# Performance work log

Hardware: AMD Instinct MI355X
Metric: run time of the kernel (lower is better)

Reference implementation:

```python
import jax, jax.numpy as jnp
import numpy as np

NUM_HEADS = 16
D_ATT = 64


def setup_inputs() -> dict:
    key = jax.random.key(0)
    ks = jax.random.split(key, 7)
    b, n, hd = 4, 2048, NUM_HEADS * 64  # input last dim = num_heads * per-head embed_dim
    Q_vec = jax.random.normal(ks[0], (b, n, hd), dtype=jnp.float32)
    K_vec = jax.random.normal(ks[1], (b, n, hd), dtype=jnp.float32)
    V_vec = jax.random.normal(ks[2], (b, n, hd), dtype=jnp.float32)
    # torch Linear weights: [out_features, in_features] = [d_attention, per_head_dim]
    W_Q = jax.random.normal(ks[3], (D_ATT, 64), dtype=jnp.float32) * 0.02
    W_K = jax.random.normal(ks[4], (D_ATT, 64), dtype=jnp.float32) * 0.02
    W_V = jax.random.normal(ks[5], (D_ATT, 64), dtype=jnp.float32) * 0.02
    mask = jax.random.bernoulli(ks[6], p=0.9, shape=(b, n))  # bool [b, n]
    return {"Q_vec": Q_vec, "K_vec": K_vec, "V_vec": V_vec,
            "W_Q": W_Q, "W_K": W_K, "W_V": W_V, "mask": mask}


def reference(Q_vec, K_vec, V_vec, W_Q, W_K, W_V, mask):
    b, n, _ = Q_vec.shape
    h = NUM_HEADS
    scaling = 1.0 / np.sqrt(D_ATT).astype(np.float32)

    def split_heads(x):  # b n (h d) -> b h n d
        return x.reshape(b, n, h, -1).transpose(0, 2, 1, 3)

    # Linear applied per-head (weights are [out, in]; y = x @ W^T)
    q = split_heads(Q_vec) @ W_Q.T  # [b,h,n,D_ATT]
    k = split_heads(K_vec) @ W_K.T
    v = split_heads(V_vec) @ W_V.T

    dots = jnp.einsum('bhid,bhjd->bhij', q, k) * scaling  # [b,h,n,n]
    pair_mask = mask[:, None, :] & mask[:, :, None]       # [b,n,n]
    mask_value = -jnp.finfo(dots.dtype).max
    dots = jnp.where(pair_mask[:, None, :, :], dots, mask_value)
    attn = jax.nn.softmax(dots, axis=-1)
    out = jnp.einsum('bhij,bhjd->bhid', attn, v)          # [b,h,n,D_ATT]
    return out.transpose(0, 2, 1, 3).reshape(b, n, h * D_ATT)
```

## Files before the change

kernel.cpp:

```cpp
#include <hip/hip_runtime.h>

#define B_  4
#define N_  2048
#define H_  16
#define HD_ 1024

typedef short  bf16x8 __attribute__((ext_vector_type(8)));
typedef short  bf16x4 __attribute__((ext_vector_type(4)));
typedef float  f32x4  __attribute__((ext_vector_type(4)));

static __device__ __forceinline__ unsigned short f2bf(float f) {
    unsigned int u = __builtin_bit_cast(unsigned int, f);
    return (unsigned short)((u + 0x8000u) >> 16);
}
static __device__ __forceinline__ unsigned f2bf2pack(float lo, float hi) {
    unsigned a = __builtin_bit_cast(unsigned, lo) + 0x8000u;
    unsigned b = __builtin_bit_cast(unsigned, hi) + 0x8000u;
    return __builtin_amdgcn_perm(b, a, 0x07060302u);
}

__global__ __launch_bounds__(256) void wconv_kernel(
    const float* __restrict__ WQ, const float* __restrict__ WK,
    const float* __restrict__ WV, unsigned short* __restrict__ wbf)
{
    const int p = blockIdx.x;
    const float* W = (p == 0) ? WQ : (p == 1) ? WK : WV;
    const float scl = (p == 0) ? 0.180336880f : 1.f;
    const int t = threadIdx.x;
    const float* src = W + t * 16;
    unsigned short* dst = wbf + p * 4096 + t * 16;
    float4 f[4];
    #pragma unroll
    for (int i = 0; i < 4; ++i) f[i] = *reinterpret_cast<const float4*>(src + i * 4);
    uint4 o0, o1;
    o0.x = f2bf2pack(f[0].x * scl, f[0].y * scl);
    o0.y = f2bf2pack(f[0].z * scl, f[0].w * scl);
    o0.z = f2bf2pack(f[1].x * scl, f[1].y * scl);
    o0.w = f2bf2pack(f[1].z * scl, f[1].w * scl);
    o1.x = f2bf2pack(f[2].x * scl, f[2].y * scl);
    o1.y = f2bf2pack(f[2].z * scl, f[2].w * scl);
    o1.z = f2bf2pack(f[3].x * scl, f[3].y * scl);
    o1.w = f2bf2pack(f[3].z * scl, f[3].w * scl);
    *reinterpret_cast<uint4*>(dst)     = o0;
    *reinterpret_cast<uint4*>(dst + 8) = o1;
}

__global__ __launch_bounds__(256) void proj_kernel(
    const float* __restrict__ Qv, const float* __restrict__ Kv,
    const float* __restrict__ Vv, const unsigned short* __restrict__ wbf,
    unsigned short* __restrict__ qs, unsigned short* __restrict__ ks,
    unsigned short* __restrict__ vt)
{
    __shared__ __align__(16) unsigned short sb[64][72];

    const int tid  = threadIdx.x;
    const int wq   = tid >> 6;
    const int lane = tid & 63;
    const int l15  = lane & 15;
    const int quad = lane >> 4;

    const int i0 = blockIdx.x * 64;
    const int h  = blockIdx.y;
    const int bz = blockIdx.z;
    const int b  = bz / 3;
    const int p  = bz - b * 3;

    const size_t bh = (size_t)b * H_ + h;
    const float* inp = ((p == 0) ? Qv : (p == 1) ? Kv : Vv)
                       + ((size_t)b * N_ + i0) * HD_ + h * 64;

    const unsigned short* wb = wbf + p * 4096;
    bf16x8 bw[4][2];
    #pragma unroll
    for (int t = 0; t < 4; ++t)
        #pragma unroll
        for (int kh = 0; kh < 2; ++kh)
            bw[t][kh] = *reinterpret_cast<const bf16x8*>(wb + (t * 16 + l15) * 64 + kh * 32 + quad * 8);

    const float* xp = inp + (size_t)(wq * 16 + l15) * HD_;
    bf16x8 ax[2];
    #pragma unroll
    for (int kh = 0; kh < 2; ++kh) {
        float4 f0 = *reinterpret_cast<const float4*>(xp + kh * 32 + quad * 8);
        float4 f1 = *reinterpret_cast<const float4*>(xp + kh * 32 + quad * 8 + 4);
        uint4 u = uint4{f2bf2pack(f0.x, f0.y), f2bf2pack(f0.z, f0.w),
                        f2bf2pack(f1.x, f1.y), f2bf2pack(f1.z, f1.w)};
        ax[kh] = __builtin_bit_cast(bf16x8, u);
    }

    f32x4 C[4];
    #pragma unroll
    for (int t = 0; t < 4; ++t) {
        C[t] = f32x4{0.f, 0.f, 0.f, 0.f};
        #pragma unroll
        for (int kh = 0; kh < 2; ++kh)
            C[t] = __builtin_amdgcn_mfma_f32_16x16x32_bf16(ax[kh], bw[t][kh], C[t], 0, 0, 0);
    }

    if (p < 2) {
        #pragma unroll
        for (int t = 0; t < 4; ++t)
            #pragma unroll
            for (int r = 0; r < 4; ++r)
                sb[wq * 16 + quad * 4 + r][t * 16 + l15] = f2bf(C[t][r]);
        __syncthreads();
        unsigned short* dst = ((p == 0) ? qs : ks) + ((size_t)bh * N_ + i0) * 64;
        #pragma unroll
        for (int v = 0; v < 2; ++v) {
            int idx = tid + v * 256;
            int row = idx >> 3, c0 = (idx & 7) * 8;
            *reinterpret_cast<uint4*>(dst + (size_t)row * 64 + c0) =
                *reinterpret_cast<const uint4*>(&sb[row][c0]);
        }
    } else {
        #pragma unroll
        for (int t = 0; t < 4; ++t) {
            uint2 u;
            u.x = f2bf2pack(C[t][0], C[t][1]);
            u.y = f2bf2pack(C[t][2], C[t][3]);
            *reinterpret_cast<uint2*>(&sb[t * 16 + l15][wq * 16 + quad * 4]) = u;
        }
        __syncthreads();
        unsigned short* vdst = vt + (size_t)bh * 64 * N_ + i0;
        #pragma unroll
        for (int v = 0; v < 2; ++v) {
            int idx = tid + v * 256;
            int d = idx >> 3, c0 = (idx & 7) * 8;
            *reinterpret_cast<uint4*>(vdst + (size_t)d * N_ + c0) =
                *reinterpret_cast<const uint4*>(&sb[d][c0]);
        }
    }
}

__global__ __launch_bounds__(256, 2) void attn_kernel(
    const unsigned short* __restrict__ qs, const unsigned short* __restrict__ ks,
    const unsigned short* __restrict__ vt, const int* __restrict__ maskp,
    float* __restrict__ out)
{
    __shared__ __align__(16) unsigned short Ks[64][72];
    __shared__ __align__(16) unsigned short Vt[64][68];
    __shared__ float kb[64];

    const int tid  = threadIdx.x;
    const int w    = tid >> 6;
    const int lane = tid & 63;
    const int l15  = lane & 15;
    const int quad = lane >> 4;

    const int i0 = blockIdx.x * 256;
    const int bh = blockIdx.y;
    const int b  = bh >> 4;
    const int h  = bh & 15;
    const int qrow0 = i0 + w * 64;

    bf16x8 aq[4][2];
    float  qm[4];
    #pragma unroll
    for (int rt = 0; rt < 4; ++rt) {
        const unsigned short* qrow = qs + ((size_t)bh * N_ + qrow0 + rt * 16 + l15) * 64;
        aq[rt][0] = *reinterpret_cast<const bf16x8*>(qrow + quad * 8);
        aq[rt][1] = *reinterpret_cast<const bf16x8*>(qrow + 32 + quad * 8);
        qm[rt] = maskp[b * N_ + qrow0 + rt * 16 + l15] ? 1.f : 0.f;
    }

    bf16x8 aones;
    #pragma unroll
    for (int j = 0; j < 8; ++j) aones[j] = (short)0x3F80;

    f32x4 O[4][4];
    f32x4 L[4];
    #pragma unroll
    for (int rt = 0; rt < 4; ++rt) {
        L[rt] = f32x4{0.f, 0.f, 0.f, 0.f};
        #pragma unroll
        for (int c = 0; c < 4; ++c) O[rt][c] = f32x4{0.f, 0.f, 0.f, 0.f};
    }

    const unsigned short* kbase = ks + (size_t)bh * N_ * 64;
    const unsigned short* vbase = vt + (size_t)bh * 64 * N_;

    for (int kv0 = 0; kv0 < N_; kv0 += 64) {
        __syncthreads();
        #pragma unroll
        for (int it = 0; it < 2; ++it) {
            int idx = tid + it * 256;
            int r = idx >> 3, g = idx & 7;
            *reinterpret_cast<uint4*>(&Ks[r][g * 8]) =
                *reinterpret_cast<const uint4*>(kbase + (size_t)(kv0 + r) * 64 + g * 8);
        }
        #pragma unroll
        for (int it = 0; it < 4; ++it) {
            int idx = tid + it * 256;
            int r = idx >> 4, g2 = idx & 15;
            *reinterpret_cast<uint2*>(&Vt[r][g2 * 4]) =
                *reinterpret_cast<const uint2*>(vbase + (size_t)r * N_ + kv0 + g2 * 4);
        }
        if (tid < 64) kb[tid] = maskp[b * N_ + kv0 + tid] ? 0.f : -1e30f;
        __syncthreads();

        bf16x8 ak[4][2];
        #pragma unroll
        for (int ct = 0; ct < 4; ++ct)
            #pragma unroll
            for (int kh = 0; kh < 2; ++kh)
                ak[ct][kh] = *reinterpret_cast<const bf16x8*>(&Ks[ct * 16 + l15][kh * 32 + quad * 8]);

        bf16x8 av[4][2];
        #pragma unroll
        for (int ct = 0; ct < 4; ++ct)
            #pragma unroll
            for (int kh = 0; kh < 2; ++kh) {
                bf16x4 lo = *reinterpret_cast<const bf16x4*>(&Vt[ct * 16 + l15][kh * 32 + quad * 4]);
                bf16x4 hi = *reinterpret_cast<const bf16x4*>(&Vt[ct * 16 + l15][kh * 32 + 16 + quad * 4]);
                av[ct][kh] = bf16x8{lo[0], lo[1], lo[2], lo[3], hi[0], hi[1], hi[2], hi[3]};
            }

        f32x4 kbv[4];
        #pragma unroll
        for (int ct = 0; ct < 4; ++ct)
            kbv[ct] = *reinterpret_cast<const f32x4*>(&kb[ct * 16 + quad * 4]);

        #pragma unroll
        for (int rt = 0; rt < 4; ++rt) {
            f32x4 S[4];
            #pragma unroll
            for (int ct = 0; ct < 4; ++ct) {
                S[ct] = kbv[ct];
                #pragma unroll
                for (int kh = 0; kh < 2; ++kh)
                    S[ct] = __builtin_amdgcn_mfma_f32_16x16x32_bf16(ak[ct][kh], aq[rt][kh], S[ct], 0, 0, 0);
            }
            unsigned pk[4][2];
            #pragma unroll
            for (int ct = 0; ct < 4; ++ct) {
                float e0 = __builtin_amdgcn_exp2f(S[ct][0] * qm[rt]);
                float e1 = __builtin_amdgcn_exp2f(S[ct][1] * qm[rt]);
                float e2 = __builtin_amdgcn_exp2f(S[ct][2] * qm[rt]);
                float e3 = __builtin_amdgcn_exp2f(S[ct][3] * qm[rt]);
                pk[ct][0] = f2bf2pack(e0, e1);
                pk[ct][1] = f2bf2pack(e2, e3);
            }
            bf16x8 ap[2];
            #pragma unroll
            for (int kh = 0; kh < 2; ++kh) {
                uint4 u = uint4{pk[2 * kh][0], pk[2 * kh][1], pk[2 * kh + 1][0], pk[2 * kh + 1][1]};
                ap[kh] = __builtin_bit_cast(bf16x8, u);
            }
            #pragma unroll
            for (int kh = 0; kh < 2; ++kh)
                L[rt] = __builtin_amdgcn_mfma_f32_16x16x32_bf16(aones, ap[kh], L[rt], 0, 0, 0);
            #pragma unroll
            for (int ct = 0; ct < 4; ++ct)
                #pragma unroll
                for (int kh = 0; kh < 2; ++kh)
                    O[rt][ct] = __builtin_amdgcn_mfma_f32_16x16x32_bf16(av[ct][kh], ap[kh], O[rt][ct], 0, 0, 0);
        }
    }

    #pragma unroll
    for (int rt = 0; rt < 4; ++rt) {
        float inv = 1.f / L[rt][0];
        float* orow = out + ((size_t)b * N_ + qrow0 + rt * 16 + l15) * HD_ + h * 64 + quad * 4;
        #pragma unroll
        for (int ct = 0; ct < 4; ++ct)
            #pragma unroll
            for (int r = 0; r < 4; ++r)
                orow[ct * 16 + r] = O[rt][ct][r] * inv;
    }
}

extern "C" void kernel_launch(void* const* d_in, const int* in_sizes, int n_in,
                              void* d_out, int out_size, void* d_ws, size_t ws_size,
                              hipStream_t stream)
{
    const float* Qv  = (const float*)d_in[0];
    const float* Kv  = (const float*)d_in[1];
    const float* Vv  = (const float*)d_in[2];
    const float* WQ  = (const float*)d_in[3];
    const float* WK  = (const float*)d_in[4];
    const float* WV  = (const float*)d_in[5];
    const int*   msk = (const int*)d_in[6];
    float* out = (float*)d_out;

    const size_t per = (size_t)B_ * H_ * N_ * 64;
    unsigned short* qsb = (unsigned short*)d_ws;
    unsigned short* ksb = qsb + per;
    unsigned short* vtb = ksb + per;
    unsigned short* wbf = vtb + per;

    wconv_kernel<<<dim3(3), 256, 0, stream>>>(WQ, WK, WV, wbf);
    proj_kernel<<<dim3(N_ / 64, H_, B_ * 3), 256, 0, stream>>>(Qv, Kv, Vv, wbf, qsb, ksb, vtb);
    attn_kernel<<<dim3(N_ / 256, B_ * H_), 256, 0, stream>>>(qsb, ksb, vtb, msk, out);
}
```

Measured before the change: 238.1 us.

## Load K/V fragments directly from global memory, drop LDS staging and barriers

The attention kernel no longer stages K, V and mask tiles in shared memory. Each wave reads its MFMA operands straight from global memory, relying on L2/cache reuse across the four waves. V is written by the projection kernel in a fragment-ready tiled layout so each lane can load a contiguous bf16x8. The mask bias is precomputed once in the weight-conversion kernel, and blocks are remapped so all blocks of a head share one XCD's L2. Occupancy bounds are relaxed. Removing the barriers lowers sync overhead, but per-wave global reads are duplicated and depend on cache hits.

After: 260.8 us. 1.1x slower.

```diff
diff --git a/kernel.cpp b/kernel.cpp
--- a/kernel.cpp
+++ b/kernel.cpp
@@ -21,12 +21,21 @@
 
 __global__ __launch_bounds__(256) void wconv_kernel(
     const float* __restrict__ WQ, const float* __restrict__ WK,
-    const float* __restrict__ WV, unsigned short* __restrict__ wbf)
+    const float* __restrict__ WV, const int* __restrict__ maskp,
+    unsigned short* __restrict__ wbf, float* __restrict__ mb)
 {
     const int p = blockIdx.x;
+    const int t = threadIdx.x;
+    if (p == 3) {
+        #pragma unroll
+        for (int i = 0; i < 32; ++i) {
+            int idx = i * 256 + t;
+            mb[idx] = maskp[idx] ? 0.f : -1e30f;
+        }
+        return;
+    }
     const float* W = (p == 0) ? WQ : (p == 1) ? WK : WV;
     const float scl = (p == 0) ? 0.180336880f : 1.f;
-    const int t = threadIdx.x;
     const float* src = W + t * 16;
     unsigned short* dst = wbf + p * 4096 + t * 16;
     float4 f[4];
@@ -113,42 +122,35 @@
                 *reinterpret_cast<const uint4*>(&sb[row][c0]);
         }
     } else {
+        unsigned short* vf = vt + (size_t)bh * 64 * N_ + (size_t)blockIdx.x * 4096;
         #pragma unroll
         for (int t = 0; t < 4; ++t) {
             uint2 u;
             u.x = f2bf2pack(C[t][0], C[t][1]);
             u.y = f2bf2pack(C[t][2], C[t][3]);
-            *reinterpret_cast<uint2*>(&sb[t * 16 + l15][wq * 16 + quad * 4]) = u;
-        }
-        __syncthreads();
-        unsigned short* vdst = vt + (size_t)bh * 64 * N_ + i0;
-        #pragma unroll
-        for (int v = 0; v < 2; ++v) {
-            int idx = tid + v * 256;
-            int d = idx >> 3, c0 = (idx & 7) * 8;
-            *reinterpret_cast<uint4*>(vdst + (size_t)d * N_ + c0) =
-                *reinterpret_cast<const uint4*>(&sb[d][c0]);
-        }
-    }
-}
-
-__global__ __launch_bounds__(256, 2) void attn_kernel(
+            *reinterpret_cast<uint2*>(vf + ((t * 2 + (wq >> 1)) * 16 + l15) * 32
+                                         + quad * 8 + (wq & 1) * 4) = u;
+        }
+    }
+}
+
+__global__ __launch_bounds__(256) void attn_kernel(
     const unsigned short* __restrict__ qs, const unsigned short* __restrict__ ks,
     const unsigned short* __restrict__ vt, const int* __restrict__ maskp,
-    float* __restrict__ out)
-{
-    __shared__ __align__(16) unsigned short Ks[64][72];
-    __shared__ __align__(16) unsigned short Vt[64][68];
-    __shared__ float kb[64];
-
+    const float* __restrict__ mb, float* __restrict__ out)
+{
     const int tid  = threadIdx.x;
     const int w    = tid >> 6;
     const int lane = tid & 63;
     const int l15  = lane & 15;
     const int quad = lane >> 4;
 
-    const int i0 = blockIdx.x * 256;
-    const int bh = blockIdx.y;
+    const int lin  = blockIdx.y * gridDim.x + blockIdx.x;
+    const int xcd  = lin & 7;
+    const int bh   = xcd * 8 + (lin >> 6);
+    const int xblk = (lin >> 3) & 7;
+
+    const int i0 = xblk * 256;
     const int b  = bh >> 4;
     const int h  = bh & 15;
     const int qrow0 = i0 + w * 64;
@@ -177,48 +179,31 @@
     }
 
     const unsigned short* kbase = ks + (size_t)bh * N_ * 64;
-    const unsigned short* vbase = vt + (size_t)bh * 64 * N_;
+    const unsigned short* vfb   = vt + (size_t)bh * 64 * N_;
+    const float* mbase = mb + b * N_;
 
     for (int kv0 = 0; kv0 < N_; kv0 += 64) {
-        __syncthreads();
-        #pragma unroll
-        for (int it = 0; it < 2; ++it) {
-            int idx = tid + it * 256;
-            int r = idx >> 3, g = idx & 7;
-            *reinterpret_cast<uint4*>(&Ks[r][g * 8]) =
-                *reinterpret_cast<const uint4*>(kbase + (size_t)(kv0 + r) * 64 + g * 8);
-        }
-        #pragma unroll
-        for (int it = 0; it < 4; ++it) {
-            int idx = tid + it * 256;
-            int r = idx >> 4, g2 = idx & 15;
-            *reinterpret_cast<uint2*>(&Vt[r][g2 * 4]) =
-                *reinterpret_cast<const uint2*>(vbase + (size_t)r * N_ + kv0 + g2 * 4);
-        }
-        if (tid < 64) kb[tid] = maskp[b * N_ + kv0 + tid] ? 0.f : -1e30f;
-        __syncthreads();
-
         bf16x8 ak[4][2];
         #pragma unroll
         for (int ct = 0; ct < 4; ++ct)
             #pragma unroll
             for (int kh = 0; kh < 2; ++kh)
-                ak[ct][kh] = *reinterpret_cast<const bf16x8*>(&Ks[ct * 16 + l15][kh * 32 + quad * 8]);
-
+                ak[ct][kh] = *reinterpret_cast<const bf16x8*>(
+                    kbase + (size_t)(kv0 + ct * 16 + l15) * 64 + kh * 32 + quad * 8);
+
+        const unsigned short* vf = vfb + (size_t)(kv0 >> 6) * 4096;
         bf16x8 av[4][2];
         #pragma unroll
         for (int ct = 0; ct < 4; ++ct)
             #pragma unroll
-            for (int kh = 0; kh < 2; ++kh) {
-                bf16x4 lo = *reinterpret_cast<const bf16x4*>(&Vt[ct * 16 + l15][kh * 32 + quad * 4]);
-                bf16x4 hi = *reinterpret_cast<const bf16x4*>(&Vt[ct * 16 + l15][kh * 32 + 16 + quad * 4]);
-                av[ct][kh] = bf16x8{lo[0], lo[1], lo[2], lo[3], hi[0], hi[1], hi[2], hi[3]};
-            }
+            for (int kh = 0; kh < 2; ++kh)
+                av[ct][kh] = *reinterpret_cast<const bf16x8*>(
+                    vf + ((ct * 2 + kh) * 16 + l15) * 32 + quad * 8);
 
         f32x4 kbv[4];
         #pragma unroll
         for (int ct = 0; ct < 4; ++ct)
-            kbv[ct] = *reinterpret_cast<const f32x4*>(&kb[ct * 16 + quad * 4]);
+            kbv[ct] = *reinterpret_cast<const f32x4*>(mbase + kv0 + ct * 16 + quad * 4);
 
         #pragma unroll
         for (int rt = 0; rt < 4; ++rt) {
@@ -287,8 +272,9 @@
     unsigned short* ksb = qsb + per;
     unsigned short* vtb = ksb + per;
     unsigned short* wbf = vtb + per;
-
-    wconv_kernel<<<dim3(3), 256, 0, stream>>>(WQ, WK, WV, wbf);
+    float*          mbf = (float*)(wbf + 3 * 4096);
+
+    wconv_kernel<<<dim3(4), 256, 0, stream>>>(WQ, WK, WV, msk, wbf, mbf);
     proj_kernel<<<dim3(N_ / 64, H_, B_ * 3), 256, 0, stream>>>(Qv, Kv, Vv, wbf, qsb, ksb, vtb);
-    attn_kernel<<<dim3(N_ / 256, B_ * H_), 256, 0, stream>>>(qsb, ksb, vtb, msk, out);
-}
+    attn_kernel<<<dim3(N_ / 256, B_ * H_), 256, 0, stream>>>(qsb, ksb, vtb, msk, mbf, out);
+}
```
